# Kernel tuning notes

Measured on AMD Instinct MI355X. Metric: run time of the kernel, lower is better.

## Reference

```python
import jax, jax.numpy as jnp
import numpy as np

N_SUP, D = 4096, 128
N_CLASSES, SHOTS = 128, 32          # balanced episode: N_SUP = N_CLASSES * SHOTS
N_QUERY = 65536
N_BOOT = 8                          # num_bootstrap_samples


def setup_inputs() -> dict:
    key = jax.random.key(0)
    k_sup, k_q, k_boot = jax.random.split(key, 3)
    support_set_repr = jax.random.normal(k_sup, (N_SUP, D), dtype=jnp.float32)
    # balanced, sorted labels: class c owns contiguous block [c*SHOTS, (c+1)*SHOTS)
    support_labels = (jnp.arange(N_SUP, dtype=jnp.int32) // SHOTS).astype(jnp.int32)
    query_set_repr = jax.random.normal(k_q, (N_QUERY, D), dtype=jnp.float32)
    # externalized torch.randint(0, num_samples, (B, num_samples)) per class
    bootstrap_indices = jax.random.randint(
        k_boot, (N_BOOT, N_CLASSES, SHOTS), 0, SHOTS, dtype=jnp.int32)
    return {
        "support_set_repr": support_set_repr,
        "support_labels": support_labels,
        "query_set_repr": query_set_repr,
        "bootstrap_indices": bootstrap_indices,
    }


def reference(support_set_repr, support_labels, query_set_repr, bootstrap_indices):
    B, C, S = bootstrap_indices.shape
    d = support_set_repr.shape[-1]
    # labels are sorted & balanced (arange // SHOTS), so per-class gather == reshape
    class_repr = support_set_repr.reshape(C, S, d)              # [C, S, D]
    # fused bootstrap gather: [B, C, S, D]
    boot = jnp.take_along_axis(class_repr[None], bootstrap_indices[..., None], axis=2)
    protos = boot.mean(axis=2)                                   # [B, C, D]
    # cdist(q, protos, p=2) via ||q||^2 + ||p||^2 - 2 q.p
    q2 = jnp.sum(query_set_repr * query_set_repr, axis=-1)       # [NQ]
    p2 = jnp.sum(protos * protos, axis=-1)                       # [B, C]
    qp = jnp.einsum('qd,bcd->bqc', query_set_repr, protos)       # [B, NQ, C]
    d2 = q2[None, :, None] + p2[:, None, :] - 2.0 * qp
    dists = jnp.sqrt(jnp.maximum(d2, 0.0))                       # [B, NQ, C]
    # logits = mean over bootstraps of -dists
    return -dists.mean(axis=0)                                   # [NQ, C]
```

## Files before the change

kernel.cpp:

```cpp
#include <hip/hip_runtime.h>


#define DIM   128
#define NCLS  128
#define SHOTS 32
#define NB    8
#define NQ    65536

using short8 = __attribute__((ext_vector_type(8))) short;
using f32x4  = __attribute__((ext_vector_type(4))) float;

__device__ __forceinline__ unsigned short f2bf(float x) {
  union { float f; unsigned u; } v; v.f = x;
  unsigned r = v.u + 0x7fffu + ((v.u >> 16) & 1u);
  return (unsigned short)(r >> 16);
}

__device__ __forceinline__ float fast_sqrt(float x) {
#if __has_builtin(__builtin_amdgcn_sqrtf)
  return __builtin_amdgcn_sqrtf(x);
#else
  return sqrtf(x);
#endif
}

__global__ __launch_bounds__(128) void proto_kernel(
    const float* __restrict__ sup, const int* __restrict__ bidx,
    unsigned short* __restrict__ pfrag, float* __restrict__ p2) {
  int bc = blockIdx.x;
  int c  = bc & (NCLS - 1);
  int d  = threadIdx.x;
  __shared__ int   sidx[SHOTS];
  __shared__ float wsum[2];
  if (d < SHOTS) sidx[d] = bidx[bc * SHOTS + d];
  __syncthreads();
  float acc = 0.f;
  const float* base = sup + c * SHOTS * DIM + d;
  #pragma unroll
  for (int s = 0; s < SHOTS; ++s) acc += base[sidx[s] * DIM];
  float proto = acc * (1.0f / 32.0f);

  int b     = bc >> 7;
  int ct    = c >> 4, l15c = c & 15;
  int kiter = d >> 5, quad = (d >> 3) & 3, j = d & 7;
  int lane  = l15c + (quad << 4);
  int slot  = (b * 8 + ct) * 4 + kiter;
  pfrag[slot * 512 + lane * 8 + j] = f2bf(proto * -0.03125f);

  float sq = proto * proto;
  #pragma unroll
  for (int off = 32; off > 0; off >>= 1) sq += __shfl_down(sq, off, 64);
  if ((d & 63) == 0) wsum[d >> 6] = sq;
  __syncthreads();
  if (d == 0) p2[bc] = (wsum[0] + wsum[1]) * (1.0f / 64.0f);
}

__global__ __launch_bounds__(256) void dist_kernel(
    const float* __restrict__ q, const uint4* __restrict__ pfrag,
    const float* __restrict__ p2, float* __restrict__ out) {
  int tid  = threadIdx.x;
  int w    = tid >> 6, lane = tid & 63;
  int l15  = lane & 15, quad = lane >> 4;
  int q0   = blockIdx.x << 5;

  short8 af[2][4];
  float  q2row[2];
  #pragma unroll
  for (int mt2 = 0; mt2 < 2; ++mt2) {
    int row = q0 + mt2 * 16 + l15;
    const float* qr = q + (size_t)row * DIM + quad * 8;
    float s = 0.f;
    #pragma unroll
    for (int k = 0; k < 4; ++k) {
      float4 x0 = *reinterpret_cast<const float4*>(qr + k * 32);
      float4 x1 = *reinterpret_cast<const float4*>(qr + k * 32 + 4);
      s += x0.x*x0.x + x0.y*x0.y + x0.z*x0.z + x0.w*x0.w
         + x1.x*x1.x + x1.y*x1.y + x1.z*x1.z + x1.w*x1.w;
      short8 a;
      a[0] = (short)f2bf(x0.x); a[1] = (short)f2bf(x0.y);
      a[2] = (short)f2bf(x0.z); a[3] = (short)f2bf(x0.w);
      a[4] = (short)f2bf(x1.x); a[5] = (short)f2bf(x1.y);
      a[6] = (short)f2bf(x1.z); a[7] = (short)f2bf(x1.w);
      af[mt2][k] = a;
    }
    s += __shfl_xor(s, 16, 64);
    s += __shfl_xor(s, 32, 64);
    q2row[mt2] = s * (1.0f / 64.0f);
  }

  f32x4 q2r[2];
  #pragma unroll
  for (int mt2 = 0; mt2 < 2; ++mt2)
    #pragma unroll
    for (int r = 0; r < 4; ++r)
      q2r[mt2][r] = __shfl(q2row[mt2], quad * 4 + r, 64);

  float p2v[NB][2];
  #pragma unroll
  for (int b = 0; b < NB; ++b)
    #pragma unroll
    for (int jj = 0; jj < 2; ++jj)
      p2v[b][jj] = p2[b * NCLS + (w * 2 + jj) * 16 + l15];

  f32x4 oacc[2][2];
  #pragma unroll
  for (int i = 0; i < 2; ++i)
    #pragma unroll
    for (int jj = 0; jj < 2; ++jj)
      oacc[i][jj] = (f32x4){0.f, 0.f, 0.f, 0.f};

  uint4 bufX[8], bufY[8];

  #define LOAD_B(BUF, B)                                                      \
    {                                                                         \
      _Pragma("unroll")                                                       \
      for (int jj = 0; jj < 2; ++jj) {                                        \
        int ct = w * 2 + jj;                                                  \
        const uint4* bp = pfrag + (size_t)(((B) * 8 + ct) * 4) * 64 + lane;   \
        _Pragma("unroll")                                                     \
        for (int k = 0; k < 4; ++k) BUF[jj * 4 + k] = bp[k * 64];             \
      }                                                                       \
    }

  #define COMPUTE_B(BUF, B)                                                   \
    {                                                                         \
      _Pragma("unroll")                                                       \
      for (int jj = 0; jj < 2; ++jj) {                                        \
        f32x4 qp0, qp1;                                                       \
        _Pragma("unroll")                                                     \
        for (int r = 0; r < 4; ++r) {                                         \
          qp0[r] = q2r[0][r] + p2v[B][jj];                                    \
          qp1[r] = q2r[1][r] + p2v[B][jj];                                    \
        }                                                                     \
        _Pragma("unroll")                                                     \
        for (int k = 0; k < 4; ++k) {                                         \
          short8 bfk = __builtin_bit_cast(short8, BUF[jj * 4 + k]);           \
          qp0 = __builtin_amdgcn_mfma_f32_16x16x32_bf16(af[0][k], bfk, qp0, 0, 0, 0); \
          qp1 = __builtin_amdgcn_mfma_f32_16x16x32_bf16(af[1][k], bfk, qp1, 0, 0, 0); \
        }                                                                     \
        _Pragma("unroll")                                                     \
        for (int r = 0; r < 4; ++r) {                                         \
          oacc[0][jj][r] += fast_sqrt(fmaxf(qp0[r], 0.0f));                   \
          oacc[1][jj][r] += fast_sqrt(fmaxf(qp1[r], 0.0f));                   \
        }                                                                     \
      }                                                                       \
    }

  LOAD_B(bufX, 0)
  #pragma unroll 1
  for (int i = 0; i < NB; i += 2) {
    LOAD_B(bufY, i + 1)
    COMPUTE_B(bufX, i)
    LOAD_B(bufX, (i + 2) & (NB - 1))
    COMPUTE_B(bufY, i + 1)
  }
  #undef LOAD_B
  #undef COMPUTE_B

  #pragma unroll
  for (int mt2 = 0; mt2 < 2; ++mt2)
    #pragma unroll
    for (int jj = 0; jj < 2; ++jj) {
      int col = (w * 2 + jj) * 16 + l15;
      #pragma unroll
      for (int r = 0; r < 4; ++r) {
        int row = q0 + mt2 * 16 + quad * 4 + r;
        out[(size_t)row * NCLS + col] = -oacc[mt2][jj][r];
      }
    }
}

extern "C" void kernel_launch(void* const* d_in, const int* in_sizes, int n_in,
                              void* d_out, int out_size, void* d_ws, size_t ws_size,
                              hipStream_t stream) {
  const float* sup   = (const float*)d_in[0];
  const float* query = (const float*)d_in[2];
  const int*   bidx  = (const int*)d_in[3];
  float* out = (float*)d_out;

  unsigned short* pfrag = (unsigned short*)d_ws;
  float* p2 = (float*)((char*)d_ws + (size_t)NB * NCLS * DIM * 2);

  proto_kernel<<<NB * NCLS, 128, 0, stream>>>(sup, bidx, pfrag, p2);
  dist_kernel<<<NQ / 32, 256, 0, stream>>>(query, (const uint4*)pfrag, p2, out);
}
```

Baseline: 121.2 us.

## Stage query tile through LDS once per block instead of per-wave loads

Each block now cooperatively loads its 32-row query tile once, computes row norms with a small shuffle reduction, and writes bf16 MFMA A-fragments into padded shared memory that all four waves then read. Previously every wave re-read and re-converted the full tile from global memory, quadrupling load and conversion work. Conversion uses packed bf16 intrinsics. The cost is an LDS round trip and a block barrier before compute starts.

```diff
diff --git a/kernel.cpp b/kernel.cpp
--- a/kernel.cpp
+++ b/kernel.cpp
@@ -1,4 +1,5 @@
 #include <hip/hip_runtime.h>
+#include <hip/hip_bf16.h>
 
 
 #define DIM   128
@@ -14,6 +15,16 @@
   union { float f; unsigned u; } v; v.f = x;
   unsigned r = v.u + 0x7fffu + ((v.u >> 16) & 1u);
   return (unsigned short)(r >> 16);
+}
+
+__device__ __forceinline__ short8 pack8_bf16(float4 a, float4 b) {
+  __hip_bfloat162 p0 = __float22bfloat162_rn(make_float2(a.x, a.y));
+  __hip_bfloat162 p1 = __float22bfloat162_rn(make_float2(a.z, a.w));
+  __hip_bfloat162 p2 = __float22bfloat162_rn(make_float2(b.x, b.y));
+  __hip_bfloat162 p3 = __float22bfloat162_rn(make_float2(b.z, b.w));
+  union { __hip_bfloat162 h[4]; short8 s; } u;
+  u.h[0] = p0; u.h[1] = p1; u.h[2] = p2; u.h[3] = p3;
+  return u.s;
 }
 
 __device__ __forceinline__ float fast_sqrt(float x) {
@@ -55,6 +66,8 @@
   if (d == 0) p2[bc] = (wsum[0] + wsum[1]) * (1.0f / 64.0f);
 }
 
+#define SLOT_STRIDE 520
+
 __global__ __launch_bounds__(256) void dist_kernel(
     const float* __restrict__ q, const uint4* __restrict__ pfrag,
     const float* __restrict__ p2, float* __restrict__ out) {
@@ -63,37 +76,47 @@
   int l15  = lane & 15, quad = lane >> 4;
   int q0   = blockIdx.x << 5;
 
+  __shared__ unsigned short aflds[8 * SLOT_STRIDE];
+  __shared__ float q2s[32];
+
+  {
+    int rloc  = w * 8 + (lane >> 3);
+    int chunk = lane & 7;
+    const float* src = q + (size_t)(q0 + rloc) * DIM + chunk * 16;
+    float4 x0 = *reinterpret_cast<const float4*>(src);
+    float4 x1 = *reinterpret_cast<const float4*>(src + 4);
+    float4 x2 = *reinterpret_cast<const float4*>(src + 8);
+    float4 x3 = *reinterpret_cast<const float4*>(src + 12);
+    float s = x0.x*x0.x + x0.y*x0.y + x0.z*x0.z + x0.w*x0.w
+            + x1.x*x1.x + x1.y*x1.y + x1.z*x1.z + x1.w*x1.w
+            + x2.x*x2.x + x2.y*x2.y + x2.z*x2.z + x2.w*x2.w
+            + x3.x*x3.x + x3.y*x3.y + x3.z*x3.z + x3.w*x3.w;
+    s += __shfl_down(s, 4, 8);
+    s += __shfl_down(s, 2, 8);
+    s += __shfl_down(s, 1, 8);
+    if (chunk == 0) q2s[rloc] = s;
+
+    int mt = rloc >> 4, m = rloc & 15, i = chunk >> 1, h = chunk & 1;
+    unsigned short* base = &aflds[(mt * 4 + i) * SLOT_STRIDE];
+    *reinterpret_cast<short8*>(&base[((h * 2 + 0) * 16 + m) * 8]) = pack8_bf16(x0, x1);
+    *reinterpret_cast<short8*>(&base[((h * 2 + 1) * 16 + m) * 8]) = pack8_bf16(x2, x3);
+  }
+  __syncthreads();
+
   short8 af[2][4];
-  float  q2row[2];
-  #pragma unroll
-  for (int mt2 = 0; mt2 < 2; ++mt2) {
-    int row = q0 + mt2 * 16 + l15;
-    const float* qr = q + (size_t)row * DIM + quad * 8;
-    float s = 0.f;
-    #pragma unroll
-    for (int k = 0; k < 4; ++k) {
-      float4 x0 = *reinterpret_cast<const float4*>(qr + k * 32);
-      float4 x1 = *reinterpret_cast<const float4*>(qr + k * 32 + 4);
-      s += x0.x*x0.x + x0.y*x0.y + x0.z*x0.z + x0.w*x0.w
-         + x1.x*x1.x + x1.y*x1.y + x1.z*x1.z + x1.w*x1.w;
-      short8 a;
-      a[0] = (short)f2bf(x0.x); a[1] = (short)f2bf(x0.y);
-      a[2] = (short)f2bf(x0.z); a[3] = (short)f2bf(x0.w);
-      a[4] = (short)f2bf(x1.x); a[5] = (short)f2bf(x1.y);
-      a[6] = (short)f2bf(x1.z); a[7] = (short)f2bf(x1.w);
-      af[mt2][k] = a;
-    }
-    s += __shfl_xor(s, 16, 64);
-    s += __shfl_xor(s, 32, 64);
-    q2row[mt2] = s * (1.0f / 64.0f);
-  }
+  #pragma unroll
+  for (int mt = 0; mt < 2; ++mt)
+    #pragma unroll
+    for (int k = 0; k < 4; ++k)
+      af[mt][k] = *reinterpret_cast<const short8*>(
+          &aflds[(mt * 4 + k) * SLOT_STRIDE + lane * 8]);
 
   f32x4 q2r[2];
   #pragma unroll
-  for (int mt2 = 0; mt2 < 2; ++mt2)
+  for (int mt = 0; mt < 2; ++mt)
     #pragma unroll
     for (int r = 0; r < 4; ++r)
-      q2r[mt2][r] = __shfl(q2row[mt2], quad * 4 + r, 64);
+      q2r[mt][r] = q2s[mt * 16 + quad * 4 + r] * (1.0f / 64.0f);
 
   float p2v[NB][2];
   #pragma unroll
```

Measured after the change: 112.9 us. 6.8% less time.
